# Optimization experiments

Hardware: AMD Instinct MI355X
Metric: run time of the kernel (lower is better)

## Reference

```python
import jax, jax.numpy as jnp
import numpy as np

N, E = 20000, 320000
NF, EF = 4, 4
HID, HEADS, MODEL_HID = 128, 4, 128


def _p(key, shape, scale=0.1):
    return scale * jax.random.normal(key, shape, dtype=jnp.float32)


def setup_inputs() -> dict:
    key = jax.random.key(0)
    ks = jax.random.split(key, 32)
    x = jax.random.normal(ks[0], (N, NF), dtype=jnp.float32)
    src = jax.random.randint(ks[1], (E,), 0, N)
    off = jax.random.randint(ks[2], (E,), 1, N)
    dst = (src + off) % N  # no self-loops (PyG removes then re-adds them)
    edge_index = jnp.stack([src, dst]).astype(jnp.int64)
    edge_attr = jax.random.uniform(ks[3], (E, EF), dtype=jnp.float32)
    d = dict(x=x, edge_index=edge_index, edge_attr=edge_attr)
    # input_proj
    d['Wp'] = _p(ks[4], (NF, HID)); d['bp'] = jnp.zeros((HID,), jnp.float32)
    # GAT layer 1: in=HID, heads=HEADS, out=HID, concat
    d['W1'] = _p(ks[5], (HID, HEADS * HID)); d['We1'] = _p(ks[6], (EF, HEADS * HID))
    d['as1'] = _p(ks[7], (HEADS, HID)); d['ad1'] = _p(ks[8], (HEADS, HID)); d['ae1'] = _p(ks[9], (HEADS, HID))
    d['b1'] = jnp.zeros((HEADS * HID,), jnp.float32)
    d['g1'] = jnp.ones((HEADS * HID,), jnp.float32); d['be1'] = jnp.zeros((HEADS * HID,), jnp.float32)
    # GAT layer 2: in=HEADS*HID, heads=1, out=HID, mean
    d['W2'] = _p(ks[10], (HEADS * HID, HID)); d['We2'] = _p(ks[11], (EF, HID))
    d['as2'] = _p(ks[12], (1, HID)); d['ad2'] = _p(ks[13], (1, HID)); d['ae2'] = _p(ks[14], (1, HID))
    d['b2'] = jnp.zeros((HID,), jnp.float32)
    d['g2'] = jnp.ones((HID,), jnp.float32); d['be2'] = jnp.zeros((HID,), jnp.float32)
    # output proj + importance scorer
    d['Wo'] = _p(ks[15], (HID, MODEL_HID)); d['bo'] = jnp.zeros((MODEL_HID,), jnp.float32)
    d['Wi'] = _p(ks[16], (MODEL_HID, 1)); d['bi'] = jnp.zeros((1,), jnp.float32)
    return d


def _layer_norm(x, g, b, eps=1e-5):
    mu = x.mean(-1, keepdims=True)
    v = ((x - mu) ** 2).mean(-1, keepdims=True)
    return (x - mu) * jax.lax.rsqrt(v + eps) * g + b


def _segment_softmax(logits, seg, num):
    m = jax.ops.segment_max(logits, seg, num_segments=num)
    e = jnp.exp(logits - m[seg])
    d = jax.ops.segment_sum(e, seg, num_segments=num)
    return e / d[seg]


def _forward(x, edge_index, edge_attr, Wp, bp, W1, We1, as1, ad1, ae1, b1, g1, be1,
             W2, We2, as2, ad2, ae2, b2, g2, be2, Wo, bo, Wi, bi):
    n = x.shape[0]
    src, dst = edge_index[0], edge_index[1]
    e = edge_attr.shape[0]
    # add_self_loops with fill_value='mean': self-loop attr = mean of incoming edge_attr
    deg = jax.ops.segment_sum(jnp.ones((e,), edge_attr.dtype), dst, num_segments=n)
    loop_attr = jax.ops.segment_sum(edge_attr, dst, num_segments=n) / jnp.maximum(deg, 1.0)[:, None]
    loops = jnp.arange(n)
    src_f = jnp.concatenate([src, loops])
    dst_f = jnp.concatenate([dst, loops])
    ea = jnp.concatenate([edge_attr, loop_attr], axis=0)  # [E+N, EF]

    def gat(h, W, We, a_s, a_d, a_e, bias, heads, out_c, concat):
        xh = (h @ W).reshape(n, heads, out_c)                 # [N,H,C]
        eh = (ea @ We).reshape(-1, heads, out_c)              # [E+N,H,C]
        al_s = (xh * a_s).sum(-1)                             # [N,H]
        al_d = (xh * a_d).sum(-1)                             # [N,H]
        al_e = (eh * a_e).sum(-1)                             # [E+N,H]
        logits = jax.nn.leaky_relu(al_s[src_f] + al_d[dst_f] + al_e, negative_slope=0.2)
        alpha = _segment_softmax(logits, dst_f, n)            # [E+N,H]
        out = jax.ops.segment_sum(xh[src_f] * alpha[..., None], dst_f, num_segments=n)
        out = out.reshape(n, heads * out_c) if concat else out.mean(axis=1)
        return out + bias, alpha

    h = x @ Wp + bp
    h, _ = gat(h, W1, We1, as1, ad1, ae1, b1, HEADS, HID, True)
    h = jax.nn.elu(_layer_norm(h, g1, be1))  # dropout is a no-op in eval
    h, edge_attention = gat(h, W2, We2, as2, ad2, ae2, b2, 1, HID, False)
    h = _layer_norm(h, g2, be2)
    emb = h @ Wo + bo
    importance = jax.nn.sigmoid(emb @ Wi + bi).squeeze(-1)
    return emb, edge_attention, importance


def reference(x, edge_index, edge_attr, Wp, bp, W1, We1, as1, ad1, ae1, b1, g1, be1,
              W2, We2, as2, ad2, ae2, b2, g2, be2, Wo, bo, Wi, bi):
    return _forward(x, edge_index, edge_attr, Wp, bp, W1, We1, as1, ad1, ae1, b1, g1, be1,
                    W2, We2, as2, ad2, ae2, b2, g2, be2, Wo, bo, Wi, bi)
```

## Files before the change

### kernel.cpp

```cpp
#include <hip/hip_runtime.h>
#include <math.h>
#include <stdint.h>

#define N_NODES 20000
#define N_EDGES 320000
#define EN_TOT  340000
#define CAP     768

typedef __attribute__((ext_vector_type(8))) _Float16 half8v;
typedef __attribute__((ext_vector_type(4))) float float4v;

__device__ __forceinline__ ushort f2h(float f) {
    _Float16 h = (_Float16)f;
    return __builtin_bit_cast(ushort, h);
}
__device__ __forceinline__ float h2f(ushort s) {
    return (float)__builtin_bit_cast(_Float16, s);
}

__global__ void k_deg(const int* __restrict__ dst, int* __restrict__ degi) {
    int e = blockIdx.x * 256 + threadIdx.x;
    if (e >= N_EDGES) return;
    atomicAdd(&degi[dst[e]], 1);
}

__global__ __launch_bounds__(1024) void k_scan(const int* __restrict__ degi, int* __restrict__ offsets,
                                               const float* __restrict__ We1, const float* __restrict__ ae1,
                                               const float* __restrict__ We2, const float* __restrict__ ae2,
                                               float* __restrict__ M1, float* __restrict__ m2) {
    __shared__ int s[1024];
    int t = threadIdx.x;
    int n0 = t * 20;
    int tot = 0;
    for (int i = 0; i < 20; i++) {
        int n = n0 + i;
        if (n < N_NODES) tot += degi[n] + 1;
    }
    s[t] = tot;
    __syncthreads();
    for (int off = 1; off < 1024; off <<= 1) {
        int v = (t >= off) ? s[t - off] : 0;
        __syncthreads();
        s[t] += v;
        __syncthreads();
    }
    int run = s[t] - tot;
    for (int i = 0; i < 20; i++) {
        int n = n0 + i;
        if (n < N_NODES) {
            offsets[n] = run;
            run += degi[n] + 1;
        }
    }
    if (t == 1023) offsets[N_NODES] = s[1023];
    if (t < 16) {
        int f = t >> 2, h = t & 3;
        float acc = 0.f;
        for (int c = 0; c < 128; c++) acc += We1[f * 512 + h * 128 + c] * ae1[h * 128 + c];
        M1[f * 4 + h] = acc;
    } else if (t < 20) {
        int f = t - 16;
        float acc = 0.f;
        for (int c = 0; c < 128; c++) acc += We2[f * 128 + c] * ae2[c];
        m2[f] = acc;
    }
}

__global__ void k_fill(const int* __restrict__ src, const int* __restrict__ dst,
                       const int* __restrict__ offsets, int* __restrict__ cursor,
                       int2* __restrict__ csr_se) {
    int i = blockIdx.x * 256 + threadIdx.x;
    if (i >= EN_TOT) return;
    int d, sidx, eid;
    if (i < N_EDGES) { d = dst[i]; sidx = src[i]; eid = i; }
    else { int n = i - N_EDGES; d = n; sidx = n; eid = N_EDGES + n; }
    int pos = offsets[d] + atomicAdd(&cursor[d], 1);
    csr_se[pos] = make_int2(sidx, eid);
}

__global__ __launch_bounds__(256) void k_loopattr(const int* __restrict__ offsets,
                                                  const int2* __restrict__ csr_se,
                                                  const float* __restrict__ eattr,
                                                  float* __restrict__ loopattr) {
    int wv = threadIdx.x >> 6, l = threadIdx.x & 63;
    int n = blockIdx.x * 4 + wv;
    if (n >= N_NODES) return;
    int start = offsets[n], end = offsets[n + 1];
    float sx = 0.f, sy = 0.f, sz = 0.f, sw = 0.f;
    for (int p = start + l; p < end; p += 64) {
        int eid = csr_se[p].y;
        if (eid < N_EDGES) {
            float4 e = *(const float4*)&eattr[(size_t)eid * 4];
            sx += e.x; sy += e.y; sz += e.z; sw += e.w;
        }
    }
    for (int off = 32; off; off >>= 1) {
        sx += __shfl_down(sx, off);
        sy += __shfl_down(sy, off);
        sz += __shfl_down(sz, off);
        sw += __shfl_down(sw, off);
    }
    if (l == 0) {
        float inv = 1.0f / fmaxf((float)(end - start - 1), 1.0f);
        float4 o;
        o.x = sx * inv; o.y = sy * inv; o.z = sz * inv; o.w = sw * inv;
        *(float4*)&loopattr[(size_t)n * 4] = o;
    }
}

__global__ void k_prep(const float* __restrict__ W1, const float* __restrict__ W2,
                       const float* __restrict__ Wo, ushort* __restrict__ W1T,
                       ushort* __restrict__ W2T, ushort* __restrict__ WoT) {
    int i = blockIdx.x * 256 + threadIdx.x;
    if (i < 512 * 128) {
        int nn = i >> 7, kk = i & 127;
        W1T[i] = f2h(W1[kk * 512 + nn]);
    } else if (i < 2 * 512 * 128) {
        int j = i - 512 * 128;
        int nn = j >> 9, kk = j & 511;
        W2T[j] = f2h(W2[kk * 128 + nn]);
    } else if (i < 2 * 512 * 128 + 128 * 128) {
        int j = i - 2 * 512 * 128;
        int nn = j >> 7, kk = j & 127;
        WoT[j] = f2h(Wo[kk * 128 + nn]);
    }
}

__global__ __launch_bounds__(256) void k_proj(const float* __restrict__ x, const float* __restrict__ Wp,
                                              const float* __restrict__ bp, ushort* __restrict__ h0h) {
    int tid = threadIdx.x;
    int n = blockIdx.x * 2 + (tid >> 7);
    int c = tid & 127;
    float acc = bp[c];
#pragma unroll
    for (int f = 0; f < 4; f++) acc += x[n * 4 + f] * Wp[f * 128 + c];
    h0h[(size_t)n * 128 + c] = f2h(acc);
}

__global__ __launch_bounds__(256) void k_gemm_hf(const ushort* __restrict__ A, const ushort* __restrict__ BT,
                                                 float* __restrict__ Cf, ushort* __restrict__ Ch,
                                                 int M, int Nn, int K, const float* __restrict__ bias) {
    __shared__ ushort As[64 * 64];
    __shared__ ushort Bs[128 * 64];
    const int tid = threadIdx.x;
    const int lane = tid & 63, wid = tid >> 6;
    const int m0 = blockIdx.x * 64, n0 = blockIdx.y * 128;
    float4v acc[4][2];
#pragma unroll
    for (int i = 0; i < 4; i++)
#pragma unroll
        for (int j = 0; j < 2; j++) acc[i][j] = (float4v){0.f, 0.f, 0.f, 0.f};

    for (int k0 = 0; k0 < K; k0 += 64) {
        __syncthreads();
#pragma unroll
        for (int i = 0; i < 2; i++) {
            int c = tid + i * 256;
            int row = c >> 3, sl = c & 7;
            int off = row * 128 + ((sl ^ (row & 7)) << 4);
            uint4 va = make_uint4(0u, 0u, 0u, 0u);
            if (m0 + row < M) va = *(const uint4*)&A[(size_t)(m0 + row) * K + k0 + sl * 8];
            *(uint4*)((char*)As + off) = va;
        }
#pragma unroll
        for (int i = 0; i < 4; i++) {
            int c = tid + i * 256;
            int row = c >> 3, sl = c & 7;
            int off = row * 128 + ((sl ^ (row & 7)) << 4);
            uint4 vb = *(const uint4*)&BT[(size_t)(n0 + row) * K + k0 + sl * 8];
            *(uint4*)((char*)Bs + off) = vb;
        }
        __syncthreads();
#pragma unroll
        for (int kk = 0; kk < 2; kk++) {
            half8v af[4], bq[2];
            int sl = kk * 4 + (lane >> 4);
#pragma unroll
            for (int mi = 0; mi < 4; mi++) {
                int row = (lane & 15) + mi * 16;
                af[mi] = *(const half8v*)((const char*)As + row * 128 + ((sl ^ (row & 7)) << 4));
            }
#pragma unroll
            for (int ni = 0; ni < 2; ni++) {
                int row = wid * 32 + ni * 16 + (lane & 15);
                bq[ni] = *(const half8v*)((const char*)Bs + row * 128 + ((sl ^ (row & 7)) << 4));
            }
#pragma unroll
            for (int mi = 0; mi < 4; mi++)
#pragma unroll
                for (int ni = 0; ni < 2; ni++)
                    acc[mi][ni] = __builtin_amdgcn_mfma_f32_16x16x32_f16(af[mi], bq[ni], acc[mi][ni], 0, 0, 0);
        }
    }
#pragma unroll
    for (int mi = 0; mi < 4; mi++) {
#pragma unroll
        for (int j = 0; j < 4; j++) {
            int row = m0 + mi * 16 + ((lane >> 4) << 2) + j;
            if (row < M) {
#pragma unroll
                for (int ni = 0; ni < 2; ni++) {
                    int col = n0 + wid * 32 + ni * 16 + (lane & 15);
                    float v = acc[mi][ni][j];
                    if (bias) v += bias[col];
                    if (Cf) Cf[(size_t)row * Nn + col] = v;
                    if (Ch) Ch[(size_t)row * Nn + col] = f2h(v);
                }
            }
        }
    }
}

__global__ __launch_bounds__(256) void k_ald1(const ushort* __restrict__ xhh, const float* __restrict__ as1,
                                              const float* __restrict__ ad1, float* __restrict__ als,
                                              float* __restrict__ ald) {
    int n = blockIdx.x;
    int w = threadIdx.x >> 6, l = threadIdx.x & 63;
    uint v = *(const uint*)&xhh[(size_t)n * 512 + w * 128 + l * 2];
    float f0 = h2f((ushort)(v & 0xffffu));
    float f1 = h2f((ushort)(v >> 16));
    float2 a = *(const float2*)&as1[w * 128 + l * 2];
    float2 b = *(const float2*)&ad1[w * 128 + l * 2];
    float ps = f0 * a.x + f1 * a.y, pd = f0 * b.x + f1 * b.y;
    for (int off = 32; off; off >>= 1) { ps += __shfl_down(ps, off); pd += __shfl_down(pd, off); }
    if (l == 0) { als[n * 4 + w] = ps; ald[n * 4 + w] = pd; }
}

__global__ __launch_bounds__(256) void k_ald2(const ushort* __restrict__ xh2h, const float* __restrict__ as2,
                                              const float* __restrict__ ad2, float* __restrict__ als,
                                              float* __restrict__ ald) {
    int w = threadIdx.x >> 6, l = threadIdx.x & 63;
    int n = blockIdx.x * 4 + w;
    if (n >= N_NODES) return;
    uint v = *(const uint*)&xh2h[(size_t)n * 128 + l * 2];
    float f0 = h2f((ushort)(v & 0xffffu));
    float f1 = h2f((ushort)(v >> 16));
    float2 a = *(const float2*)&as2[l * 2];
    float2 b = *(const float2*)&ad2[l * 2];
    float ps = f0 * a.x + f1 * a.y, pd = f0 * b.x + f1 * b.y;
    for (int off = 32; off; off >>= 1) { ps += __shfl_down(ps, off); pd += __shfl_down(pd, off); }
    if (l == 0) { als[n] = ps; ald[n] = pd; }
}

__global__ __launch_bounds__(128) void k_agg1(const int* __restrict__ offsets, const int2* __restrict__ csr_se,
                                              const float* __restrict__ eattr, const float* __restrict__ loopattr,
                                              const float* __restrict__ als, const float* __restrict__ aldv,
                                              const float* __restrict__ M1, const ushort* __restrict__ xhh,
                                              const float* __restrict__ b1, const float* __restrict__ g1,
                                              const float* __restrict__ be1, ushort* __restrict__ h1h) {
    int n = blockIdx.x;
    int start = offsets[n];
    int cnt = offsets[n + 1] - start;
    int tid = threadIdx.x;
    int lane = tid & 63, wv = tid >> 6;
    __shared__ float Lc[CAP][4];
    __shared__ int   sSrc[CAP];
    __shared__ float mws[2][4], sws[2][4];
    __shared__ float mh[4], shv[4];
    __shared__ float wred[2], wred2[2];

    int hh = tid & 3;
    float aldn = aldv[n * 4 + hh];
    float c0 = M1[0 * 4 + hh], c1 = M1[1 * 4 + hh], c2 = M1[2 * 4 + hh], c3 = M1[3 * 4 + hh];
    float m = -1e30f, s = 0.f;
    for (int j = tid >> 2; j < cnt; j += 32) {
        int p = start + j;
        int2 se = csr_se[p];
        const float* eap = (se.y < N_EDGES) ? &eattr[(size_t)se.y * 4] : &loopattr[(size_t)(se.y - N_EDGES) * 4];
        float4 e4 = *(const float4*)eap;
        float l = als[se.x * 4 + hh] + aldn + e4.x * c0 + e4.y * c1 + e4.z * c2 + e4.w * c3;
        l = (l >= 0.f) ? l : 0.2f * l;
        Lc[j][hh] = l;
        if (hh == 0) sSrc[j] = se.x;
        float mn = fmaxf(m, l);
        s = s * __expf(m - mn) + __expf(l - mn);
        m = mn;
    }
#pragma unroll
    for (int off = 4; off < 64; off <<= 1) {
        float mo = __shfl_xor(m, off), so = __shfl_xor(s, off);
        float mn = fmaxf(m, mo);
        s = s * __expf(m - mn) + so * __expf(mo - mn);
        m = mn;
    }
    if (lane < 4) { mws[wv][lane] = m; sws[wv][lane] = s; }
    __syncthreads();
    if (tid < 4) {
        float M0 = mws[0][tid], S0 = sws[0][tid];
        float M1b = mws[1][tid], S1 = sws[1][tid];
        float mn = fmaxf(M0, M1b);
        float S = S0 * __expf(M0 - mn) + S1 * __expf(M1b - mn);
        mh[tid] = mn; shv[tid] = 1.0f / S;
    }
    __syncthreads();
    int tot = cnt * 4;
    for (int idx = tid; idx < tot; idx += 128) {
        int j = idx >> 2, h = idx & 3;
        Lc[j][h] = __expf(Lc[j][h] - mh[h]) * shv[h];
    }
    __syncthreads();

    float acc0 = 0.f, acc1 = 0.f, acc2 = 0.f, acc3 = 0.f;
    int hg = tid >> 5;
    uint ch = (uint)tid * 4u;
    int j = 0;
    for (; j + 4 <= cnt; j += 4) {
        float a0 = Lc[j][hg], a1 = Lc[j + 1][hg], a2 = Lc[j + 2][hg], a3 = Lc[j + 3][hg];
        uint o0 = ((uint)sSrc[j] << 9) + ch;
        uint o1 = ((uint)sSrc[j + 1] << 9) + ch;
        uint o2 = ((uint)sSrc[j + 2] << 9) + ch;
        uint o3 = ((uint)sSrc[j + 3] << 9) + ch;
        uint2 v0 = *(const uint2*)&xhh[o0];
        uint2 v1 = *(const uint2*)&xhh[o1];
        uint2 v2 = *(const uint2*)&xhh[o2];
        uint2 v3 = *(const uint2*)&xhh[o3];
        acc0 += a0 * h2f((ushort)(v0.x & 0xffffu)) + a1 * h2f((ushort)(v1.x & 0xffffu))
              + a2 * h2f((ushort)(v2.x & 0xffffu)) + a3 * h2f((ushort)(v3.x & 0xffffu));
        acc1 += a0 * h2f((ushort)(v0.x >> 16)) + a1 * h2f((ushort)(v1.x >> 16))
              + a2 * h2f((ushort)(v2.x >> 16)) + a3 * h2f((ushort)(v3.x >> 16));
        acc2 += a0 * h2f((ushort)(v0.y & 0xffffu)) + a1 * h2f((ushort)(v1.y & 0xffffu))
              + a2 * h2f((ushort)(v2.y & 0xffffu)) + a3 * h2f((ushort)(v3.y & 0xffffu));
        acc3 += a0 * h2f((ushort)(v0.y >> 16)) + a1 * h2f((ushort)(v1.y >> 16))
              + a2 * h2f((ushort)(v2.y >> 16)) + a3 * h2f((ushort)(v3.y >> 16));
    }
    for (; j < cnt; j++) {
        float a = Lc[j][hg];
        uint2 v = *(const uint2*)&xhh[((uint)sSrc[j] << 9) + ch];
        acc0 += a * h2f((ushort)(v.x & 0xffffu));
        acc1 += a * h2f((ushort)(v.x >> 16));
        acc2 += a * h2f((ushort)(v.y & 0xffffu));
        acc3 += a * h2f((ushort)(v.y >> 16));
    }

    float4 bb = *(const float4*)&b1[tid * 4];
    float v0 = acc0 + bb.x, v1 = acc1 + bb.y, v2 = acc2 + bb.z, v3 = acc3 + bb.w;
    float s4 = v0 + v1 + v2 + v3;
#pragma unroll
    for (int off = 1; off < 64; off <<= 1) s4 += __shfl_xor(s4, off);
    if (lane == 0) wred[wv] = s4;
    __syncthreads();
    float mu = (wred[0] + wred[1]) * (1.0f / 512.0f);
    float d0 = v0 - mu, d1 = v1 - mu, d2 = v2 - mu, d3 = v3 - mu;
    float sq = d0 * d0 + d1 * d1 + d2 * d2 + d3 * d3;
#pragma unroll
    for (int off = 1; off < 64; off <<= 1) sq += __shfl_xor(sq, off);
    if (lane == 0) wred2[wv] = sq;
    __syncthreads();
    float rstd = rsqrtf((wred2[0] + wred2[1]) * (1.0f / 512.0f) + 1e-5f);
    float4 gg = *(const float4*)&g1[tid * 4];
    float4 ee = *(const float4*)&be1[tid * 4];
    float y0 = d0 * rstd * gg.x + ee.x;
    float y1 = d1 * rstd * gg.y + ee.y;
    float y2 = d2 * rstd * gg.z + ee.z;
    float y3 = d3 * rstd * gg.w + ee.w;
    y0 = (y0 > 0.f) ? y0 : (__expf(y0) - 1.0f);
    y1 = (y1 > 0.f) ? y1 : (__expf(y1) - 1.0f);
    y2 = (y2 > 0.f) ? y2 : (__expf(y2) - 1.0f);
    y3 = (y3 > 0.f) ? y3 : (__expf(y3) - 1.0f);
    uint2 o;
    o.x = (uint)f2h(y0) | ((uint)f2h(y1) << 16);
    o.y = (uint)f2h(y2) | ((uint)f2h(y3) << 16);
    *(uint2*)&h1h[(size_t)n * 512 + tid * 4] = o;
}

__global__ __launch_bounds__(64) void k_agg2(const int* __restrict__ offsets, const int2* __restrict__ csr_se,
                                             const float* __restrict__ eattr, const float* __restrict__ loopattr,
                                             const float* __restrict__ als, const float* __restrict__ aldv,
                                             const float* __restrict__ m2v, const ushort* __restrict__ xh2h,
                                             const float* __restrict__ b2, const float* __restrict__ g2,
                                             const float* __restrict__ be2, float* __restrict__ eaout,
                                             ushort* __restrict__ h2h) {
    int n = blockIdx.x;
    int start = offsets[n];
    int cnt = offsets[n + 1] - start;
    int lane = threadIdx.x;
    __shared__ float Lc[CAP];
    __shared__ int   sSrc[CAP];
    __shared__ int   sEid[CAP];

    float aldn = aldv[n];
    float c0 = m2v[0], c1 = m2v[1], c2 = m2v[2], c3 = m2v[3];
    float m = -1e30f, s = 0.f;
    for (int j = lane; j < cnt; j += 64) {
        int p = start + j;
        int2 se = csr_se[p];
        const float* eap = (se.y < N_EDGES) ? &eattr[(size_t)se.y * 4] : &loopattr[(size_t)(se.y - N_EDGES) * 4];
        float4 e4 = *(const float4*)eap;
        float l = als[se.x] + aldn + e4.x * c0 + e4.y * c1 + e4.z * c2 + e4.w * c3;
        l = (l >= 0.f) ? l : 0.2f * l;
        Lc[j] = l; sSrc[j] = se.x; sEid[j] = se.y;
        float mn = fmaxf(m, l);
        s = s * __expf(m - mn) + __expf(l - mn);
        m = mn;
    }
#pragma unroll
    for (int off = 1; off < 64; off <<= 1) {
        float mo = __shfl_xor(m, off), so = __shfl_xor(s, off);
        float mn = fmaxf(m, mo);
        s = s * __expf(m - mn) + so * __expf(mo - mn);
        m = mn;
    }
    float inv = 1.0f / s;
    for (int j = lane; j < cnt; j += 64) {
        float a = __expf(Lc[j] - m) * inv;
        Lc[j] = a;
        eaout[sEid[j]] = a;
    }
    __syncthreads();
    float acc0 = 0.f, acc1 = 0.f;
    uint ch = (uint)lane * 2u;
    int j = 0;
    for (; j + 4 <= cnt; j += 4) {
        float a0 = Lc[j], a1 = Lc[j + 1], a2 = Lc[j + 2], a3 = Lc[j + 3];
        uint v0 = *(const uint*)&xh2h[((uint)sSrc[j] << 7) + ch];
        uint v1 = *(const uint*)&xh2h[((uint)sSrc[j + 1] << 7) + ch];
        uint v2 = *(const uint*)&xh2h[((uint)sSrc[j + 2] << 7) + ch];
        uint v3 = *(const uint*)&xh2h[((uint)sSrc[j + 3] << 7) + ch];
        acc0 += a0 * h2f((ushort)(v0 & 0xffffu)) + a1 * h2f((ushort)(v1 & 0xffffu))
              + a2 * h2f((ushort)(v2 & 0xffffu)) + a3 * h2f((ushort)(v3 & 0xffffu));
        acc1 += a0 * h2f((ushort)(v0 >> 16)) + a1 * h2f((ushort)(v1 >> 16))
              + a2 * h2f((ushort)(v2 >> 16)) + a3 * h2f((ushort)(v3 >> 16));
    }
    for (; j < cnt; j++) {
        float a = Lc[j];
        uint v = *(const uint*)&xh2h[((uint)sSrc[j] << 7) + ch];
        acc0 += a * h2f((ushort)(v & 0xffffu));
        acc1 += a * h2f((ushort)(v >> 16));
    }
    float2 bb = *(const float2*)&b2[lane * 2];
    float v0 = acc0 + bb.x, v1 = acc1 + bb.y;
    float s2 = v0 + v1;
#pragma unroll
    for (int off = 1; off < 64; off <<= 1) s2 += __shfl_xor(s2, off);
    float mu = s2 * (1.0f / 128.0f);
    float d0 = v0 - mu, d1 = v1 - mu;
    float q = d0 * d0 + d1 * d1;
#pragma unroll
    for (int off = 1; off < 64; off <<= 1) q += __shfl_xor(q, off);
    float rstd = rsqrtf(q * (1.0f / 128.0f) + 1e-5f);
    float2 gg = *(const float2*)&g2[lane * 2];
    float2 ee = *(const float2*)&be2[lane * 2];
    float y0 = d0 * rstd * gg.x + ee.x;
    float y1 = d1 * rstd * gg.y + ee.y;
    uint o = (uint)f2h(y0) | ((uint)f2h(y1) << 16);
    *(uint*)&h2h[(size_t)n * 128 + lane * 2] = o;
}

__global__ __launch_bounds__(256) void k_imp(const float* __restrict__ emb, const float* __restrict__ Wi,
                                             const float* __restrict__ bi, float* __restrict__ impout) {
    int w = threadIdx.x >> 6, l = threadIdx.x & 63;
    int n = blockIdx.x * 4 + w;
    if (n >= N_NODES) return;
    const float* ep = &emb[(size_t)n * 128];
    float p = ep[l] * Wi[l] + ep[l + 64] * Wi[l + 64];
    for (int off = 32; off; off >>= 1) p += __shfl_down(p, off);
    if (l == 0) impout[n] = 1.0f / (1.0f + expf(-(p + bi[0])));
}

extern "C" void kernel_launch(void* const* d_in, const int* in_sizes, int n_in,
                              void* d_out, int out_size, void* d_ws, size_t ws_size,
                              hipStream_t stream) {
    const float* x    = (const float*)d_in[0];
    const int*   eidx = (const int*)d_in[1];
    const float* eattr= (const float*)d_in[2];
    const float* Wp   = (const float*)d_in[3];
    const float* bp   = (const float*)d_in[4];
    const float* W1   = (const float*)d_in[5];
    const float* We1  = (const float*)d_in[6];
    const float* as1  = (const float*)d_in[7];
    const float* ad1  = (const float*)d_in[8];
    const float* ae1  = (const float*)d_in[9];
    const float* b1   = (const float*)d_in[10];
    const float* g1   = (const float*)d_in[11];
    const float* be1  = (const float*)d_in[12];
    const float* W2   = (const float*)d_in[13];
    const float* We2  = (const float*)d_in[14];
    const float* as2  = (const float*)d_in[15];
    const float* ad2  = (const float*)d_in[16];
    const float* ae2  = (const float*)d_in[17];
    const float* b2   = (const float*)d_in[18];
    const float* g2   = (const float*)d_in[19];
    const float* be2  = (const float*)d_in[20];
    const float* Wo   = (const float*)d_in[21];
    const float* bo   = (const float*)d_in[22];
    const float* Wi   = (const float*)d_in[23];
    const float* bi   = (const float*)d_in[24];

    const int* src = eidx;
    const int* dst = eidx + N_EDGES;

    float* emb_out = (float*)d_out;
    float* ea_out  = emb_out + (size_t)N_NODES * 128;
    float* imp_out = ea_out + EN_TOT;

    char* w = (char*)d_ws;
    auto alloc = [&](size_t bytes) -> void* { void* p = (void*)w; w += (bytes + 255) & ~(size_t)255; return p; };
    ushort* xhh    = (ushort*)alloc((size_t)N_NODES * 512 * 2);
    ushort* h1h    = (ushort*)alloc((size_t)N_NODES * 512 * 2);
    ushort* h0h    = (ushort*)alloc((size_t)N_NODES * 128 * 2);
    ushort* xh2h   = (ushort*)alloc((size_t)N_NODES * 128 * 2);
    ushort* h2h    = (ushort*)alloc((size_t)N_NODES * 128 * 2);
    ushort* W1T    = (ushort*)alloc((size_t)512 * 128 * 2);
    ushort* W2T    = (ushort*)alloc((size_t)128 * 512 * 2);
    ushort* WoT    = (ushort*)alloc((size_t)128 * 128 * 2);
    int2*  csr_se  = (int2*)alloc((size_t)EN_TOT * 8);
    int*   offsets = (int*)alloc((size_t)(N_NODES + 1) * 4);
    int*   cursor  = (int*)alloc((size_t)N_NODES * 4);
    int*   degi    = (int*)alloc((size_t)N_NODES * 4);
    float* loopat  = (float*)alloc((size_t)N_NODES * 4 * 4);
    float* als1v   = (float*)alloc((size_t)N_NODES * 4 * 4);
    float* ald1v   = (float*)alloc((size_t)N_NODES * 4 * 4);
    float* als2v   = (float*)alloc((size_t)N_NODES * 4);
    float* ald2v   = (float*)alloc((size_t)N_NODES * 4);
    float* M1      = (float*)alloc(32 * 4);
    float* m2      = M1 + 16;

    hipMemsetAsync(degi,   0, (size_t)N_NODES * 4, stream);
    hipMemsetAsync(cursor, 0, (size_t)N_NODES * 4, stream);

    k_deg<<<(N_EDGES + 255) / 256, 256, 0, stream>>>(dst, degi);
    k_scan<<<1, 1024, 0, stream>>>(degi, offsets, We1, ae1, We2, ae2, M1, m2);
    k_fill<<<(EN_TOT + 255) / 256, 256, 0, stream>>>(src, dst, offsets, cursor, csr_se);
    k_loopattr<<<(N_NODES + 3) / 4, 256, 0, stream>>>(offsets, csr_se, eattr, loopat);
    k_prep<<<576, 256, 0, stream>>>(W1, W2, Wo, W1T, W2T, WoT);
    k_proj<<<N_NODES / 2, 256, 0, stream>>>(x, Wp, bp, h0h);

    k_gemm_hf<<<dim3((N_NODES + 63) / 64, 4), 256, 0, stream>>>(h0h, W1T, nullptr, xhh,
                                                                N_NODES, 512, 128, nullptr);
    k_ald1<<<N_NODES, 256, 0, stream>>>(xhh, as1, ad1, als1v, ald1v);
    k_agg1<<<N_NODES, 128, 0, stream>>>(offsets, csr_se, eattr, loopat, als1v, ald1v, M1,
                                        xhh, b1, g1, be1, h1h);

    k_gemm_hf<<<dim3((N_NODES + 63) / 64, 1), 256, 0, stream>>>(h1h, W2T, nullptr, xh2h,
                                                                N_NODES, 128, 512, nullptr);
    k_ald2<<<(N_NODES + 3) / 4, 256, 0, stream>>>(xh2h, as2, ad2, als2v, ald2v);
    k_agg2<<<N_NODES, 64, 0, stream>>>(offsets, csr_se, eattr, loopat, als2v, ald2v, m2,
                                       xh2h, b2, g2, be2, ea_out, h2h);

    k_gemm_hf<<<dim3((N_NODES + 63) / 64, 1), 256, 0, stream>>>(h2h, WoT, emb_out, nullptr,
                                                                N_NODES, 128, 128, bo);
    k_imp<<<(N_NODES + 3) / 4, 256, 0, stream>>>(emb_out, Wi, bi, imp_out);
}
```

Before: 238.8 us.

## Use one wavefront per node in GAT aggregation and merge small prep kernels

Both aggregation kernels now handle one node per 64-lane wavefront, two nodes per block, with per-wave shared buffers. This removes the block-wide __syncthreads and cross-wave reductions. Layer 1 loads 8 halfs per lane with uint4, and layer 2's gather loop is unrolled to 8. The loop-attribute, weight-transpose/convert and input-projection kernels are merged into one launch dispatched by block index. CAP drops from 768 to 160 so shared memory fits two nodes per block, which silently overflows if any node's in-degree plus self-loop exceeds 160.

```diff
diff --git a/kernel.cpp b/kernel.cpp
--- a/kernel.cpp
+++ b/kernel.cpp
@@ -5,7 +5,7 @@
 #define N_NODES 20000
 #define N_EDGES 320000
 #define EN_TOT  340000
-#define CAP     768
+#define CAP     160
 
 typedef __attribute__((ext_vector_type(8))) _Float16 half8v;
 typedef __attribute__((ext_vector_type(4))) float float4v;
@@ -78,63 +78,62 @@
     csr_se[pos] = make_int2(sidx, eid);
 }
 
-__global__ __launch_bounds__(256) void k_loopattr(const int* __restrict__ offsets,
-                                                  const int2* __restrict__ csr_se,
-                                                  const float* __restrict__ eattr,
-                                                  float* __restrict__ loopattr) {
-    int wv = threadIdx.x >> 6, l = threadIdx.x & 63;
-    int n = blockIdx.x * 4 + wv;
-    if (n >= N_NODES) return;
-    int start = offsets[n], end = offsets[n + 1];
-    float sx = 0.f, sy = 0.f, sz = 0.f, sw = 0.f;
-    for (int p = start + l; p < end; p += 64) {
-        int eid = csr_se[p].y;
-        if (eid < N_EDGES) {
-            float4 e = *(const float4*)&eattr[(size_t)eid * 4];
-            sx += e.x; sy += e.y; sz += e.z; sw += e.w;
-        }
-    }
-    for (int off = 32; off; off >>= 1) {
-        sx += __shfl_down(sx, off);
-        sy += __shfl_down(sy, off);
-        sz += __shfl_down(sz, off);
-        sw += __shfl_down(sw, off);
-    }
-    if (l == 0) {
-        float inv = 1.0f / fmaxf((float)(end - start - 1), 1.0f);
-        float4 o;
-        o.x = sx * inv; o.y = sy * inv; o.z = sz * inv; o.w = sw * inv;
-        *(float4*)&loopattr[(size_t)n * 4] = o;
-    }
-}
-
-__global__ void k_prep(const float* __restrict__ W1, const float* __restrict__ W2,
-                       const float* __restrict__ Wo, ushort* __restrict__ W1T,
-                       ushort* __restrict__ W2T, ushort* __restrict__ WoT) {
-    int i = blockIdx.x * 256 + threadIdx.x;
-    if (i < 512 * 128) {
-        int nn = i >> 7, kk = i & 127;
-        W1T[i] = f2h(W1[kk * 512 + nn]);
-    } else if (i < 2 * 512 * 128) {
-        int j = i - 512 * 128;
-        int nn = j >> 9, kk = j & 511;
-        W2T[j] = f2h(W2[kk * 128 + nn]);
-    } else if (i < 2 * 512 * 128 + 128 * 128) {
-        int j = i - 2 * 512 * 128;
-        int nn = j >> 7, kk = j & 127;
-        WoT[j] = f2h(Wo[kk * 128 + nn]);
-    }
-}
-
-__global__ __launch_bounds__(256) void k_proj(const float* __restrict__ x, const float* __restrict__ Wp,
+__global__ __launch_bounds__(256) void k_misc(const int* __restrict__ offsets, const int2* __restrict__ csr_se,
+                                              const float* __restrict__ eattr, float* __restrict__ loopattr,
+                                              const float* __restrict__ W1, const float* __restrict__ W2,
+                                              const float* __restrict__ Wo, ushort* __restrict__ W1T,
+                                              ushort* __restrict__ W2T, ushort* __restrict__ WoT,
+                                              const float* __restrict__ x, const float* __restrict__ Wp,
                                               const float* __restrict__ bp, ushort* __restrict__ h0h) {
+    int b = blockIdx.x;
     int tid = threadIdx.x;
-    int n = blockIdx.x * 2 + (tid >> 7);
-    int c = tid & 127;
-    float acc = bp[c];
-#pragma unroll
-    for (int f = 0; f < 4; f++) acc += x[n * 4 + f] * Wp[f * 128 + c];
-    h0h[(size_t)n * 128 + c] = f2h(acc);
+    if (b < 5000) {
+        int wv = tid >> 6, l = tid & 63;
+        int n = b * 4 + wv;
+        if (n >= N_NODES) return;
+        int start = offsets[n], end = offsets[n + 1];
+        float sx = 0.f, sy = 0.f, sz = 0.f, sw = 0.f;
+        for (int p = start + l; p < end; p += 64) {
+            int eid = csr_se[p].y;
+            if (eid < N_EDGES) {
+                float4 e = *(const float4*)&eattr[(size_t)eid * 4];
+                sx += e.x; sy += e.y; sz += e.z; sw += e.w;
+            }
+        }
+        for (int off = 32; off; off >>= 1) {
+            sx += __shfl_down(sx, off);
+            sy += __shfl_down(sy, off);
+            sz += __shfl_down(sz, off);
+            sw += __shfl_down(sw, off);
+        }
+        if (l == 0) {
+            float inv = 1.0f / fmaxf((float)(end - start - 1), 1.0f);
+            float4 o;
+            o.x = sx * inv; o.y = sy * inv; o.z = sz * inv; o.w = sw * inv;
+            *(float4*)&loopattr[(size_t)n * 4] = o;
+        }
+    } else if (b < 5576) {
+        int i = (b - 5000) * 256 + tid;
+        if (i < 512 * 128) {
+            int nn = i >> 7, kk = i & 127;
+            W1T[i] = f2h(W1[kk * 512 + nn]);
+        } else if (i < 2 * 512 * 128) {
+            int j = i - 512 * 128;
+            int nn = j >> 9, kk = j & 511;
+            W2T[j] = f2h(W2[kk * 128 + nn]);
+        } else if (i < 2 * 512 * 128 + 128 * 128) {
+            int j = i - 2 * 512 * 128;
+            int nn = j >> 7, kk = j & 127;
+            WoT[j] = f2h(Wo[kk * 128 + nn]);
+        }
+    } else {
+        int n = (b - 5576) * 2 + (tid >> 7);
+        int c = tid & 127;
+        float acc = bp[c];
+#pragma unroll
+        for (int f = 0; f < 4; f++) acc += x[n * 4 + f] * Wp[f * 128 + c];
+        h0h[(size_t)n * 128 + c] = f2h(acc);
+    }
 }
 
 __global__ __launch_bounds__(256) void k_gemm_hf(const ushort* __restrict__ A, const ushort* __restrict__ BT,
@@ -248,30 +247,27 @@
                                               const float* __restrict__ M1, const ushort* __restrict__ xhh,
                                               const float* __restrict__ b1, const float* __restrict__ g1,
                                               const float* __restrict__ be1, ushort* __restrict__ h1h) {
-    int n = blockIdx.x;
+    int wv = threadIdx.x >> 6, lane = threadIdx.x & 63;
+    int n = blockIdx.x * 2 + wv;
+    __shared__ float Lc[2][CAP][4];
+    __shared__ int   sSrc[2][CAP];
+    __shared__ float mhs[2][4], shs[2][4];
+
     int start = offsets[n];
     int cnt = offsets[n + 1] - start;
-    int tid = threadIdx.x;
-    int lane = tid & 63, wv = tid >> 6;
-    __shared__ float Lc[CAP][4];
-    __shared__ int   sSrc[CAP];
-    __shared__ float mws[2][4], sws[2][4];
-    __shared__ float mh[4], shv[4];
-    __shared__ float wred[2], wred2[2];
-
-    int hh = tid & 3;
+
+    int hh = lane & 3;
     float aldn = aldv[n * 4 + hh];
-    float c0 = M1[0 * 4 + hh], c1 = M1[1 * 4 + hh], c2 = M1[2 * 4 + hh], c3 = M1[3 * 4 + hh];
+    float c0 = M1[hh], c1 = M1[4 + hh], c2 = M1[8 + hh], c3 = M1[12 + hh];
     float m = -1e30f, s = 0.f;
-    for (int j = tid >> 2; j < cnt; j += 32) {
-        int p = start + j;
-        int2 se = csr_se[p];
+    for (int j = lane >> 2; j < cnt; j += 16) {
+        int2 se = csr_se[start + j];
         const float* eap = (se.y < N_EDGES) ? &eattr[(size_t)se.y * 4] : &loopattr[(size_t)(se.y - N_EDGES) * 4];
         float4 e4 = *(const float4*)eap;
         float l = als[se.x * 4 + hh] + aldn + e4.x * c0 + e4.y * c1 + e4.z * c2 + e4.w * c3;
         l = (l >= 0.f) ? l : 0.2f * l;
-        Lc[j][hh] = l;
-        if (hh == 0) sSrc[j] = se.x;
+        Lc[wv][j][hh] = l;
+        if (hh == 0) sSrc[wv][j] = se.x;
         float mn = fmaxf(m, l);
         s = s * __expf(m - mn) + __expf(l - mn);
         m = mn;
@@ -283,112 +279,108 @@
         s = s * __expf(m - mn) + so * __expf(mo - mn);
         m = mn;
     }
-    if (lane < 4) { mws[wv][lane] = m; sws[wv][lane] = s; }
-    __syncthreads();
-    if (tid < 4) {
-        float M0 = mws[0][tid], S0 = sws[0][tid];
-        float M1b = mws[1][tid], S1 = sws[1][tid];
-        float mn = fmaxf(M0, M1b);
-        float S = S0 * __expf(M0 - mn) + S1 * __expf(M1b - mn);
-        mh[tid] = mn; shv[tid] = 1.0f / S;
-    }
-    __syncthreads();
+    if (lane < 4) { mhs[wv][lane] = m; shs[wv][lane] = 1.0f / s; }
+
     int tot = cnt * 4;
-    for (int idx = tid; idx < tot; idx += 128) {
+    for (int idx = lane; idx < tot; idx += 64) {
         int j = idx >> 2, h = idx & 3;
-        Lc[j][h] = __expf(Lc[j][h] - mh[h]) * shv[h];
-    }
-    __syncthreads();
-
-    float acc0 = 0.f, acc1 = 0.f, acc2 = 0.f, acc3 = 0.f;
-    int hg = tid >> 5;
-    uint ch = (uint)tid * 4u;
+        Lc[wv][j][h] = __expf(Lc[wv][j][h] - mhs[wv][h]) * shs[wv][h];
+    }
+
+    float acc[8];
+#pragma unroll
+    for (int i = 0; i < 8; i++) acc[i] = 0.f;
+    int hg = lane >> 4;
+    uint ch = (uint)lane * 8u;
+    auto accum = [&](float a, uint4 v) {
+        acc[0] += a * h2f((ushort)(v.x & 0xffffu));
+        acc[1] += a * h2f((ushort)(v.x >> 16));
+        acc[2] += a * h2f((ushort)(v.y & 0xffffu));
+        acc[3] += a * h2f((ushort)(v.y >> 16));
+        acc[4] += a * h2f((ushort)(v.z & 0xffffu));
+        acc[5] += a * h2f((ushort)(v.z >> 16));
+        acc[6] += a * h2f((ushort)(v.w & 0xffffu));
+        acc[7] += a * h2f((ushort)(v.w >> 16));
+    };
     int j = 0;
     for (; j + 4 <= cnt; j += 4) {
-        float a0 = Lc[j][hg], a1 = Lc[j + 1][hg], a2 = Lc[j + 2][hg], a3 = Lc[j + 3][hg];
-        uint o0 = ((uint)sSrc[j] << 9) + ch;
-        uint o1 = ((uint)sSrc[j + 1] << 9) + ch;
-        uint o2 = ((uint)sSrc[j + 2] << 9) + ch;
-        uint o3 = ((uint)sSrc[j + 3] << 9) + ch;
-        uint2 v0 = *(const uint2*)&xhh[o0];
-        uint2 v1 = *(const uint2*)&xhh[o1];
-        uint2 v2 = *(const uint2*)&xhh[o2];
-        uint2 v3 = *(const uint2*)&xhh[o3];
-        acc0 += a0 * h2f((ushort)(v0.x & 0xffffu)) + a1 * h2f((ushort)(v1.x & 0xffffu))
-              + a2 * h2f((ushort)(v2.x & 0xffffu)) + a3 * h2f((ushort)(v3.x & 0xffffu));
-        acc1 += a0 * h2f((ushort)(v0.x >> 16)) + a1 * h2f((ushort)(v1.x >> 16))
-              + a2 * h2f((ushort)(v2.x >> 16)) + a3 * h2f((ushort)(v3.x >> 16));
-        acc2 += a0 * h2f((ushort)(v0.y & 0xffffu)) + a1 * h2f((ushort)(v1.y & 0xffffu))
-              + a2 * h2f((ushort)(v2.y & 0xffffu)) + a3 * h2f((ushort)(v3.y & 0xffffu));
-        acc3 += a0 * h2f((ushort)(v0.y >> 16)) + a1 * h2f((ushort)(v1.y >> 16))
-              + a2 * h2f((ushort)(v2.y >> 16)) + a3 * h2f((ushort)(v3.y >> 16));
+        float a0 = Lc[wv][j][hg], a1 = Lc[wv][j + 1][hg];
+        float a2 = Lc[wv][j + 2][hg], a3 = Lc[wv][j + 3][hg];
+        uint4 v0 = *(const uint4*)&xhh[((uint)sSrc[wv][j] << 9) + ch];
+        uint4 v1 = *(const uint4*)&xhh[((uint)sSrc[wv][j + 1] << 9) + ch];
+        uint4 v2 = *(const uint4*)&xhh[((uint)sSrc[wv][j + 2] << 9) + ch];
+        uint4 v3 = *(const uint4*)&xhh[((uint)sSrc[wv][j + 3] << 9) + ch];
+        accum(a0, v0); accum(a1, v1); accum(a2, v2); accum(a3, v3);
     }
     for (; j < cnt; j++) {
-        float a = Lc[j][hg];
-        uint2 v = *(const uint2*)&xhh[((uint)sSrc[j] << 9) + ch];
-        acc0 += a * h2f((ushort)(v.x & 0xffffu));
-        acc1 += a * h2f((ushort)(v.x >> 16));
-        acc2 += a * h2f((ushort)(v.y & 0xffffu));
-        acc3 += a * h2f((ushort)(v.y >> 16));
-    }
-
-    float4 bb = *(const float4*)&b1[tid * 4];
-    float v0 = acc0 + bb.x, v1 = acc1 + bb.y, v2 = acc2 + bb.z, v3 = acc3 + bb.w;
-    float s4 = v0 + v1 + v2 + v3;
-#pragma unroll
-    for (int off = 1; off < 64; off <<= 1) s4 += __shfl_xor(s4, off);
-    if (lane == 0) wred[wv] = s4;
-    __syncthreads();
-    float mu = (wred[0] + wred[1]) * (1.0f / 512.0f);
+        float a = Lc[wv][j][hg];
+        uint4 v = *(const uint4*)&xhh[((uint)sSrc[wv][j] << 9) + ch];
+        accum(a, v);
+    }
+
+    float4 ba = *(const float4*)&b1[ch];
+    float4 bb = *(const float4*)&b1[ch + 4];
+    float v0 = acc[0] + ba.x, v1 = acc[1] + ba.y, v2 = acc[2] + ba.z, v3 = acc[3] + ba.w;
+    float v4 = acc[4] + bb.x, v5 = acc[5] + bb.y, v6 = acc[6] + bb.z, v7 = acc[7] + bb.w;
+    float s8 = v0 + v1 + v2 + v3 + v4 + v5 + v6 + v7;
+#pragma unroll
+    for (int off = 1; off < 64; off <<= 1) s8 += __shfl_xor(s8, off);
+    float mu = s8 * (1.0f / 512.0f);
     float d0 = v0 - mu, d1 = v1 - mu, d2 = v2 - mu, d3 = v3 - mu;
-    float sq = d0 * d0 + d1 * d1 + d2 * d2 + d3 * d3;
+    float d4 = v4 - mu, d5 = v5 - mu, d6 = v6 - mu, d7 = v7 - mu;
+    float sq = d0 * d0 + d1 * d1 + d2 * d2 + d3 * d3 + d4 * d4 + d5 * d5 + d6 * d6 + d7 * d7;
 #pragma unroll
     for (int off = 1; off < 64; off <<= 1) sq += __shfl_xor(sq, off);
-    if (lane == 0) wred2[wv] = sq;
-    __syncthreads();
-    float rstd = rsqrtf((wred2[0] + wred2[1]) * (1.0f / 512.0f) + 1e-5f);
-    float4 gg = *(const float4*)&g1[tid * 4];
-    float4 ee = *(const float4*)&be1[tid * 4];
-    float y0 = d0 * rstd * gg.x + ee.x;
-    float y1 = d1 * rstd * gg.y + ee.y;
-    float y2 = d2 * rstd * gg.z + ee.z;
-    float y3 = d3 * rstd * gg.w + ee.w;
+    float rstd = rsqrtf(sq * (1.0f / 512.0f) + 1e-5f);
+    float4 ga = *(const float4*)&g1[ch];
+    float4 gb = *(const float4*)&g1[ch + 4];
+    float4 ea = *(const float4*)&be1[ch];
+    float4 eb = *(const float4*)&be1[ch + 4];
+    float y0 = d0 * rstd * ga.x + ea.x, y1 = d1 * rstd * ga.y + ea.y;
+    float y2 = d2 * rstd * ga.z + ea.z, y3 = d3 * rstd * ga.w + ea.w;
+    float y4 = d4 * rstd * gb.x + eb.x, y5 = d5 * rstd * gb.y + eb.y;
+    float y6 = d6 * rstd * gb.z + eb.z, y7 = d7 * rstd * gb.w + eb.w;
     y0 = (y0 > 0.f) ? y0 : (__expf(y0) - 1.0f);
     y1 = (y1 > 0.f) ? y1 : (__expf(y1) - 1.0f);
     y2 = (y2 > 0.f) ? y2 : (__expf(y2) - 1.0f);
     y3 = (y3 > 0.f) ? y3 : (__expf(y3) - 1.0f);
-    uint2 o;
+    y4 = (y4 > 0.f) ? y4 : (__expf(y4) - 1.0f);
+    y5 = (y5 > 0.f) ? y5 : (__expf(y5) - 1.0f);
+    y6 = (y6 > 0.f) ? y6 : (__expf(y6) - 1.0f);
+    y7 = (y7 > 0.f) ? y7 : (__expf(y7) - 1.0f);
+    uint4 o;
     o.x = (uint)f2h(y0) | ((uint)f2h(y1) << 16);
     o.y = (uint)f2h(y2) | ((uint)f2h(y3) << 16);
-    *(uint2*)&h1h[(size_t)n * 512 + tid * 4] = o;
-}
-
-__global__ __launch_bounds__(64) void k_agg2(const int* __restrict__ offsets, const int2* __restrict__ csr_se,
-                                             const float* __restrict__ eattr, const float* __restrict__ loopattr,
-                                             const float* __restrict__ als, const float* __restrict__ aldv,
-                                             const float* __restrict__ m2v, const ushort* __restrict__ xh2h,
-                                             const float* __restrict__ b2, const float* __restrict__ g2,
-                                             const float* __restrict__ be2, float* __restrict__ eaout,
-                                             ushort* __restrict__ h2h) {
-    int n = blockIdx.x;
+    o.z = (uint)f2h(y4) | ((uint)f2h(y5) << 16);
+    o.w = (uint)f2h(y6) | ((uint)f2h(y7) << 16);
+    *(uint4*)&h1h[(size_t)n * 512 + ch] = o;
+}
+
+__global__ __launch_bounds__(128) void k_agg2(const int* __restrict__ offsets, const int2* __restrict__ csr_se,
+                                              const float* __restrict__ eattr, const float* __restrict__ loopattr,
+                                              const float* __restrict__ als, const float* __restrict__ aldv,
+                                              const float* __restrict__ m2v, const ushort* __restrict__ xh2h,
+                                              const float* __restrict__ b2, const float* __restrict__ g2,
+                                              const float* __restrict__ be2, float* __restrict__ eaout,
+                                              ushort* __restrict__ h2h) {
+    int wv = threadIdx.x >> 6, lane = threadIdx.x & 63;
+    int n = blockIdx.x * 2 + wv;
+    __shared__ float Lc[2][CAP];
+    __shared__ int   sS[2][CAP];
+    __shared__ int   sE[2][CAP];
+
     int start = offsets[n];
     int cnt = offsets[n + 1] - start;
-    int lane = threadIdx.x;
-    __shared__ float Lc[CAP];
-    __shared__ int   sSrc[CAP];
-    __shared__ int   sEid[CAP];
-
     float aldn = aldv[n];
     float c0 = m2v[0], c1 = m2v[1], c2 = m2v[2], c3 = m2v[3];
     float m = -1e30f, s = 0.f;
     for (int j = lane; j < cnt; j += 64) {
-        int p = start + j;
-        int2 se = csr_se[p];
+        int2 se = csr_se[start + j];
         const float* eap = (se.y < N_EDGES) ? &eattr[(size_t)se.y * 4] : &loopattr[(size_t)(se.y - N_EDGES) * 4];
         float4 e4 = *(const float4*)eap;
         float l = als[se.x] + aldn + e4.x * c0 + e4.y * c1 + e4.z * c2 + e4.w * c3;
         l = (l >= 0.f) ? l : 0.2f * l;
-        Lc[j] = l; sSrc[j] = se.x; sEid[j] = se.y;
+        Lc[wv][j] = l; sS[wv][j] = se.x; sE[wv][j] = se.y;
         float mn = fmaxf(m, l);
         s = s * __expf(m - mn) + __expf(l - mn);
         m = mn;
@@ -402,32 +394,40 @@
     }
     float inv = 1.0f / s;
     for (int j = lane; j < cnt; j += 64) {
-        float a = __expf(Lc[j] - m) * inv;
-        Lc[j] = a;
-        eaout[sEid[j]] = a;
-    }
-    __syncthreads();
+        float a = __expf(Lc[wv][j] - m) * inv;
+        Lc[wv][j] = a;
+        eaout[sE[wv][j]] = a;
+    }
     float acc0 = 0.f, acc1 = 0.f;
     uint ch = (uint)lane * 2u;
     int j = 0;
-    for (; j + 4 <= cnt; j += 4) {
-        float a0 = Lc[j], a1 = Lc[j + 1], a2 = Lc[j + 2], a3 = Lc[j + 3];
-        uint v0 = *(const uint*)&xh2h[((uint)sSrc[j] << 7) + ch];
-        uint v1 = *(const uint*)&xh2h[((uint)sSrc[j + 1] << 7) + ch];
-        uint v2 = *(const uint*)&xh2h[((uint)sSrc[j + 2] << 7) + ch];
-        uint v3 = *(const uint*)&xh2h[((uint)sSrc[j + 3] << 7) + ch];
+    for (; j + 8 <= cnt; j += 8) {
+        float a0 = Lc[wv][j], a1 = Lc[wv][j + 1], a2 = Lc[wv][j + 2], a3 = Lc[wv][j + 3];
+        float a4 = Lc[wv][j + 4], a5 = Lc[wv][j + 5], a6 = Lc[wv][j + 6], a7 = Lc[wv][j + 7];
+        uint v0 = *(const uint*)&xh2h[((uint)sS[wv][j] << 7) + ch];
+        uint v1 = *(const uint*)&xh2h[((uint)sS[wv][j + 1] << 7) + ch];
+        uint v2 = *(const uint*)&xh2h[((uint)sS[wv][j + 2] << 7) + ch];
+        uint v3 = *(const uint*)&xh2h[((uint)sS[wv][j + 3] << 7) + ch];
+        uint v4 = *(const uint*)&xh2h[((uint)sS[wv][j + 4] << 7) + ch];
+        uint v5 = *(const uint*)&xh2h[((uint)sS[wv][j + 5] << 7) + ch];
+        uint v6 = *(const uint*)&xh2h[((uint)sS[wv][j + 6] << 7) + ch];
+        uint v7 = *(const uint*)&xh2h[((uint)sS[wv][j + 7] << 7) + ch];
         acc0 += a0 * h2f((ushort)(v0 & 0xffffu)) + a1 * h2f((ushort)(v1 & 0xffffu))
-              + a2 * h2f((ushort)(v2 & 0xffffu)) + a3 * h2f((ushort)(v3 & 0xffffu));
+              + a2 * h2f((ushort)(v2 & 0xffffu)) + a3 * h2f((ushort)(v3 & 0xffffu))
+              + a4 * h2f((ushort)(v4 & 0xffffu)) + a5 * h2f((ushort)(v5 & 0xffffu))
+              + a6 * h2f((ushort)(v6 & 0xffffu)) + a7 * h2f((ushort)(v7 & 0xffffu));
         acc1 += a0 * h2f((ushort)(v0 >> 16)) + a1 * h2f((ushort)(v1 >> 16))
-              + a2 * h2f((ushort)(v2 >> 16)) + a3 * h2f((ushort)(v3 >> 16));
+              + a2 * h2f((ushort)(v2 >> 16)) + a3 * h2f((ushort)(v3 >> 16))
+              + a4 * h2f((ushort)(v4 >> 16)) + a5 * h2f((ushort)(v5 >> 16))
+              + a6 * h2f((ushort)(v6 >> 16)) + a7 * h2f((ushort)(v7 >> 16));
     }
     for (; j < cnt; j++) {
-        float a = Lc[j];
-        uint v = *(const uint*)&xh2h[((uint)sSrc[j] << 7) + ch];
+        float a = Lc[wv][j];
+        uint v = *(const uint*)&xh2h[((uint)sS[wv][j] << 7) + ch];
         acc0 += a * h2f((ushort)(v & 0xffffu));
         acc1 += a * h2f((ushort)(v >> 16));
     }
-    float2 bb = *(const float2*)&b2[lane * 2];
+    float2 bb = *(const float2*)&b2[ch];
     float v0 = acc0 + bb.x, v1 = acc1 + bb.y;
     float s2 = v0 + v1;
 #pragma unroll
@@ -438,12 +438,12 @@
 #pragma unroll
     for (int off = 1; off < 64; off <<= 1) q += __shfl_xor(q, off);
     float rstd = rsqrtf(q * (1.0f / 128.0f) + 1e-5f);
-    float2 gg = *(const float2*)&g2[lane * 2];
-    float2 ee = *(const float2*)&be2[lane * 2];
+    float2 gg = *(const float2*)&g2[ch];
+    float2 ee = *(const float2*)&be2[ch];
     float y0 = d0 * rstd * gg.x + ee.x;
     float y1 = d1 * rstd * gg.y + ee.y;
     uint o = (uint)f2h(y0) | ((uint)f2h(y1) << 16);
-    *(uint*)&h2h[(size_t)n * 128 + lane * 2] = o;
+    *(uint*)&h2h[(size_t)n * 128 + ch] = o;
 }
 
 __global__ __launch_bounds__(256) void k_imp(const float* __restrict__ emb, const float* __restrict__ Wi,
@@ -521,21 +521,20 @@
     k_deg<<<(N_EDGES + 255) / 256, 256, 0, stream>>>(dst, degi);
     k_scan<<<1, 1024, 0, stream>>>(degi, offsets, We1, ae1, We2, ae2, M1, m2);
     k_fill<<<(EN_TOT + 255) / 256, 256, 0, stream>>>(src, dst, offsets, cursor, csr_se);
-    k_loopattr<<<(N_NODES + 3) / 4, 256, 0, stream>>>(offsets, csr_se, eattr, loopat);
-    k_prep<<<576, 256, 0, stream>>>(W1, W2, Wo, W1T, W2T, WoT);
-    k_proj<<<N_NODES / 2, 256, 0, stream>>>(x, Wp, bp, h0h);
+    k_misc<<<15576, 256, 0, stream>>>(offsets, csr_se, eattr, loopat, W1, W2, Wo,
+                                      W1T, W2T, WoT, x, Wp, bp, h0h);
 
     k_gemm_hf<<<dim3((N_NODES + 63) / 64, 4), 256, 0, stream>>>(h0h, W1T, nullptr, xhh,
                                                                 N_NODES, 512, 128, nullptr);
     k_ald1<<<N_NODES, 256, 0, stream>>>(xhh, as1, ad1, als1v, ald1v);
-    k_agg1<<<N_NODES, 128, 0, stream>>>(offsets, csr_se, eattr, loopat, als1v, ald1v, M1,
-                                        xhh, b1, g1, be1, h1h);
+    k_agg1<<<N_NODES / 2, 128, 0, stream>>>(offsets, csr_se, eattr, loopat, als1v, ald1v, M1,
+                                            xhh, b1, g1, be1, h1h);
 
     k_gemm_hf<<<dim3((N_NODES + 63) / 64, 1), 256, 0, stream>>>(h1h, W2T, nullptr, xh2h,
                                                                 N_NODES, 128, 512, nullptr);
     k_ald2<<<(N_NODES + 3) / 4, 256, 0, stream>>>(xh2h, as2, ad2, als2v, ald2v);
-    k_agg2<<<N_NODES, 64, 0, stream>>>(offsets, csr_se, eattr, loopat, als2v, ald2v, m2,
-                                       xh2h, b2, g2, be2, ea_out, h2h);
+    k_agg2<<<N_NODES / 2, 128, 0, stream>>>(offsets, csr_se, eattr, loopat, als2v, ald2v, m2,
+                                            xh2h, b2, g2, be2, ea_out, h2h);
 
     k_gemm_hf<<<dim3((N_NODES + 63) / 64, 1), 256, 0, stream>>>(h2h, WoT, emb_out, nullptr,
                                                                 N_NODES, 128, 128, bo);
```

New measurement: 220.5 us. 7.7% less time.
